# Optimization experiments

Hardware: AMD Instinct MI355X
Metric: run time of the kernel (lower is better)

Reference implementation:

```python
import jax, jax.numpy as jnp
import numpy as np

B, S, E, KD = 4, 2048, 1024, 1024

def setup_inputs() -> dict:
    key = jax.random.key(0)
    k1, k2, k3, k4 = jax.random.split(key, 4)
    # nn.Linear weights are [out_features, in_features]
    x = jax.random.normal(k1, (B, S, E), dtype=jnp.float32)
    W_q = jax.random.normal(k2, (KD, E), dtype=jnp.float32) * (E ** -0.5)
    W_k = jax.random.normal(k3, (KD, E), dtype=jnp.float32) * (E ** -0.5)
    W_v = jax.random.normal(k4, (E, E), dtype=jnp.float32) * (E ** -0.5)
    return {"x": x, "W_q": W_q, "W_k": W_k, "W_v": W_v}

def reference(x, W_q, W_k, W_v):
    # Projections: y = x @ W.T  (torch Linear convention)
    Q = jnp.einsum('bse,ke->bsk', x, W_q)   # [B,S,KD]
    K = jnp.einsum('bse,ke->bsk', x, W_k)   # [B,S,KD]
    V = jnp.einsum('bse,fe->bsf', x, W_v)   # [B,S,E]
    key_dim = W_q.shape[0]
    scores = jnp.einsum('bqk,bsk->bqs', Q, K) / jnp.sqrt(jnp.asarray(key_dim, x.dtype))
    S_len = x.shape[1]
    causal = jnp.tril(jnp.ones((S_len, S_len), dtype=bool))  # [S,S]
    scores = jnp.where(causal, scores, -jnp.inf)
    weights = jax.nn.softmax(scores, axis=-1)                # [B,S,S]
    out = jnp.einsum('bqs,bsf->bqf', weights, V)             # [B,S,E]
    return out
```

## Files before the change

kernel.cpp:

```cpp
#include <hip/hip_runtime.h>

typedef _Float16 f16;
typedef _Float16 f16x8 __attribute__((ext_vector_type(8)));
typedef float    f32x4 __attribute__((ext_vector_type(4)));

__device__ __forceinline__ void gld_lds16(const void* g, void* l) {
    __builtin_amdgcn_global_load_lds((__attribute__((address_space(1))) void*)g,
                                     (__attribute__((address_space(3))) void*)l,
                                     16, 0, 0);
}

#define BARRIER() do { asm volatile("" ::: "memory"); \
                       __builtin_amdgcn_s_barrier();  \
                       asm volatile("" ::: "memory"); } while (0)

template<bool STG, int VM1, int VM4>
__device__ __forceinline__ void tile256(
    f32x4 (&acc)[8][4],
    const f16* Ak0, const f16* Ak1, const f16* Bk0, const f16* Bk1,
    const f16* gAn, const f16* gBn,
    f16* lAn, f16* lBn,
    int lda, int ldb)
{
    {
        f16x8 a[4], b[4];
        #pragma unroll
        for (int mf = 0; mf < 4; mf++) a[mf] = *(const f16x8*)(Ak0 + mf * 1024);
        #pragma unroll
        for (int nf = 0; nf < 4; nf++) b[nf] = *(const f16x8*)(Bk0 + nf * 1024);
        if (STG) {
            gld_lds16(gBn,                  lBn);
            gld_lds16(gBn + (long)64 * ldb, lBn + 4096);
        }
        BARRIER();
        __builtin_amdgcn_s_setprio(1);
        #pragma unroll
        for (int mf = 0; mf < 4; mf++)
            #pragma unroll
            for (int nf = 0; nf < 4; nf++)
                acc[mf][nf] = __builtin_amdgcn_mfma_f32_16x16x32_f16(
                    a[mf], b[nf], acc[mf][nf], 0, 0, 0);
        __builtin_amdgcn_s_setprio(0);
        if (VM1 == 2)      asm volatile("s_waitcnt vmcnt(2)" ::: "memory");
        else if (VM1 == 0) asm volatile("s_waitcnt vmcnt(0)" ::: "memory");
        BARRIER();
        f16x8 a2[4];
        #pragma unroll
        for (int mf = 0; mf < 4; mf++) a2[mf] = *(const f16x8*)(Ak0 + (mf + 4) * 1024);
        if (STG) {
            gld_lds16(gBn + (long)128 * ldb, lBn + 8192);
            gld_lds16(gBn + (long)192 * ldb, lBn + 12288);
        }
        BARRIER();
        __builtin_amdgcn_s_setprio(1);
        #pragma unroll
        for (int mf = 0; mf < 4; mf++)
            #pragma unroll
            for (int nf = 0; nf < 4; nf++)
                acc[mf + 4][nf] = __builtin_amdgcn_mfma_f32_16x16x32_f16(
                    a2[mf], b[nf], acc[mf + 4][nf], 0, 0, 0);
        __builtin_amdgcn_s_setprio(0);
        BARRIER();
    }
    {
        f16x8 a[4], b[4];
        #pragma unroll
        for (int mf = 0; mf < 4; mf++) a[mf] = *(const f16x8*)(Ak1 + mf * 1024);
        #pragma unroll
        for (int nf = 0; nf < 4; nf++) b[nf] = *(const f16x8*)(Bk1 + nf * 1024);
        if (STG) {
            gld_lds16(gAn,                   lAn);
            gld_lds16(gAn + (long)128 * lda, lAn + 8192);
        }
        BARRIER();
        __builtin_amdgcn_s_setprio(1);
        #pragma unroll
        for (int mf = 0; mf < 4; mf++)
            #pragma unroll
            for (int nf = 0; nf < 4; nf++)
                acc[mf][nf] = __builtin_amdgcn_mfma_f32_16x16x32_f16(
                    a[mf], b[nf], acc[mf][nf], 0, 0, 0);
        __builtin_amdgcn_s_setprio(0);
        BARRIER();
        f16x8 a2[4];
        #pragma unroll
        for (int mf = 0; mf < 4; mf++) a2[mf] = *(const f16x8*)(Ak1 + (mf + 4) * 1024);
        if (STG) {
            gld_lds16(gAn + (long)64 * lda,  lAn + 4096);
            gld_lds16(gAn + (long)192 * lda, lAn + 12288);
        }
        BARRIER();
        __builtin_amdgcn_s_setprio(1);
        #pragma unroll
        for (int mf = 0; mf < 4; mf++)
            #pragma unroll
            for (int nf = 0; nf < 4; nf++)
                acc[mf + 4][nf] = __builtin_amdgcn_mfma_f32_16x16x32_f16(
                    a2[mf], b[nf], acc[mf + 4][nf], 0, 0, 0);
        __builtin_amdgcn_s_setprio(0);
        if (VM4 == 2)      asm volatile("s_waitcnt vmcnt(2)" ::: "memory");
        else if (VM4 == 0) asm volatile("s_waitcnt vmcnt(0)" ::: "memory");
        BARRIER();
    }
}

__global__ void __launch_bounds__(512, 2)
gemm256_k1024(const f16* __restrict__ A, const f16* __restrict__ B,
              f16* __restrict__ C, int lda, int ldb, int ldc)
{
    const int m  = (int)blockIdx.x;
    const int L  = (m & 7) * 32 + (m >> 3);
    const int i0 = (L >> 3) * 256;
    const int j0 = (L & 7) * 256;

    __shared__ f16 Lds[2 * 32768] __attribute__((aligned(16)));

    const int tid  = threadIdx.x;
    const int lane = tid & 63;
    const int wave = tid >> 6;
    const int wm = wave >> 2, wn = wave & 3;
    const int row16 = lane & 15, quad = lane >> 4;
    const int swz = row16 & 7;

    const int c0 = (quad ^ swz) * 8;
    const int c1 = ((quad + 4) ^ swz) * 8;
    const f16* A0k0 = Lds + (wm * 128 + row16) * 64 + c0;
    const f16* A0k1 = Lds + (wm * 128 + row16) * 64 + c1;
    const f16* B0k0 = Lds + 16384 + (wn * 64 + row16) * 64 + c0;
    const f16* B0k1 = Lds + 16384 + (wn * 64 + row16) * 64 + c1;

    const int srow = tid >> 3;
    const int scol = ((tid & 7) ^ (srow & 7)) * 8;
    const f16* gA = A + (long)(i0 + srow) * lda + scol;
    const f16* gB = B + (long)(j0 + srow) * ldb + scol;
    f16* lA0 = Lds + tid * 8;
    f16* lB0 = Lds + 16384 + tid * 8;
    f16* lA1 = Lds + 32768 + tid * 8;
    f16* lB1 = Lds + 32768 + 16384 + tid * 8;

    gld_lds16(gB,                   lB0);
    gld_lds16(gB + (long)64 * ldb,  lB0 + 4096);
    gld_lds16(gB + (long)128 * ldb, lB0 + 8192);
    gld_lds16(gB + (long)192 * ldb, lB0 + 12288);
    gld_lds16(gA,                   lA0);
    gld_lds16(gA + (long)128 * lda, lA0 + 8192);
    gld_lds16(gA + (long)64 * lda,  lA0 + 4096);
    gld_lds16(gA + (long)192 * lda, lA0 + 12288);

    f32x4 acc[8][4] = {};

    asm volatile("s_waitcnt vmcnt(2)" ::: "memory");
    BARRIER();

    for (int t = 0; t < 14; t += 2) {
        tile256<true, 2, 2>(acc, A0k0, A0k1, B0k0, B0k1,
                            gA + (t + 1) * 64, gB + (t + 1) * 64,
                            lA1, lB1, lda, ldb);
        tile256<true, 2, 2>(acc, A0k0 + 32768, A0k1 + 32768,
                            B0k0 + 32768, B0k1 + 32768,
                            gA + (t + 2) * 64, gB + (t + 2) * 64,
                            lA0, lB0, lda, ldb);
    }
    tile256<true, 2, 2>(acc, A0k0, A0k1, B0k0, B0k1,
                        gA + 15 * 64, gB + 15 * 64, lA1, lB1, lda, ldb);
    tile256<false, 0, -1>(acc, A0k0 + 32768, A0k1 + 32768,
                          B0k0 + 32768, B0k1 + 32768,
                          nullptr, nullptr, nullptr, nullptr, lda, ldb);

    #pragma unroll
    for (int mf = 0; mf < 8; mf++) {
        const int r0 = i0 + wm * 128 + mf * 16 + quad * 4;
        #pragma unroll
        for (int nf = 0; nf < 4; nf++) {
            const int c = j0 + wn * 64 + nf * 16 + row16;
            #pragma unroll
            for (int r = 0; r < 4; r++)
                C[(long)(r0 + r) * ldc + c] = (f16)acc[mf][nf][r];
        }
    }
}

template<typename OutT>
__device__ __forceinline__ void gemm128_body(
    const f16* __restrict__ A, const f16* __restrict__ B, OutT* __restrict__ C,
    int lda, int ldb, int ldc, int Keff, float scale, int i0, int j0)
{
    __shared__ f16 As[128 * 64] __attribute__((aligned(16)));
    __shared__ f16 Bs[64 * 64]  __attribute__((aligned(16)));

    const int tid  = threadIdx.x;
    const int lane = tid & 63;
    const int wave = tid >> 6;
    const int row16 = lane & 15;
    const int quad  = lane >> 4;
    const int swz   = row16 & 7;
    const int wr = (wave >> 1) * 64;
    const int wc = (wave & 1) * 32;

    const int srow = tid >> 3;
    const int scol = ((tid & 7) ^ (srow & 7)) * 8;
    const f16* gA = A + (long)(i0 + srow) * lda + scol;
    const f16* gB = B + (long)(j0 + srow) * ldb + scol;
    f16* lA = As + tid * 8;
    f16* lB = Bs + tid * 8;

    f32x4 acc[4][2] = {};

    for (int k0 = 0; k0 < Keff; k0 += 64) {
        gld_lds16(gA + k0,                  lA);
        gld_lds16(gA + k0 + (long)32 * lda, lA + 32 * 64);
        gld_lds16(gA + k0 + (long)64 * lda, lA + 64 * 64);
        gld_lds16(gA + k0 + (long)96 * lda, lA + 96 * 64);
        gld_lds16(gB + k0,                  lB);
        gld_lds16(gB + k0 + (long)32 * ldb, lB + 32 * 64);
        __syncthreads();

        #pragma unroll
        for (int kk = 0; kk < 2; kk++) {
            f16x8 af[4], bf[2];
            #pragma unroll
            for (int t = 0; t < 4; t++)
                af[t] = *(const f16x8*)(As + (wr + t * 16 + row16) * 64
                                           + (((kk * 4 + quad) ^ swz) * 8));
            #pragma unroll
            for (int t = 0; t < 2; t++)
                bf[t] = *(const f16x8*)(Bs + (wc + t * 16 + row16) * 64
                                           + (((kk * 4 + quad) ^ swz) * 8));
            #pragma unroll
            for (int mt = 0; mt < 4; mt++)
                #pragma unroll
                for (int nt = 0; nt < 2; nt++)
                    acc[mt][nt] = __builtin_amdgcn_mfma_f32_16x16x32_f16(
                        af[mt], bf[nt], acc[mt][nt], 0, 0, 0);
        }
        __syncthreads();
    }

    #pragma unroll
    for (int mt = 0; mt < 4; mt++) {
        const int r0 = i0 + wr + mt * 16 + quad * 4;
        #pragma unroll
        for (int nt = 0; nt < 2; nt++) {
            const int c = j0 + wc + nt * 16 + row16;
            #pragma unroll
            for (int r = 0; r < 4; r++)
                C[(long)(r0 + r) * ldc + c] = (OutT)(acc[mt][nt][r] * scale);
        }
    }
}

__global__ void __launch_bounds__(256)
gemm_vt_sc(const f16* __restrict__ xh, const f16* __restrict__ wvh,
           const f16* __restrict__ QKh, f16* __restrict__ Vt,
           f16* __restrict__ Sc)
{
    const int blk = (int)blockIdx.x;
    if (blk < 1024) {
        const int L = (blk & 7) * 128 + (blk >> 3);
        const int j = L >> 3;
        const int i = L & 7;
        gemm128_body<f16>(wvh, xh, Vt, 1024, 1024, 8192, 1024, 1.f,
                          i * 128, j * 64);
    } else {
        const int m = blk - 1024;
        const int L = (m & 7) * 136 + (m >> 3);
        const int z = L / 272;
        const int r = L - z * 272;
        int y = 0;
        while ((y + 1) * (y + 2) <= r) y++;
        const int x = r - y * (y + 1);
        const long off = (long)z * (2048L * 2048);
        gemm128_body<f16>(QKh + off, QKh + 1024 + off, Sc + off,
                          2048, 2048, 2048, 1024, 0.03125f, y * 128, x * 64);
    }
}

__global__ void __launch_bounds__(256)
gemm_pv(const f16* __restrict__ Sc, const f16* __restrict__ Vt,
        float* __restrict__ out)
{
    const int n  = (int)blockIdx.x;
    const int by = 15 - (n >> 6);
    const int rem = n & 63;
    const int x  = rem >> 2;
    const int z  = rem & 3;
    const int i0 = by * 128;
    const int Keff = i0 + 128;
    gemm128_body<float>(Sc + (long)z * (2048L * 2048),
                        Vt + (long)z * 2048,
                        out + (long)z * (2048L * 1024),
                        2048, 8192, 1024, Keff, 1.f, i0, x * 64);
}

__global__ void __launch_bounds__(256)
softmax_causal(f16* __restrict__ Sc)
{
    const int bid = (int)blockIdx.x;
    const int k = bid & 7;
    const int s = bid >> 3;
    const long b = k >> 1;
    int i;
    if (!(k & 1)) i = s;
    else          i = (s < 640) ? (1408 + s) : (1024 + (s - 640));

    f16* row = Sc + ((b * 2048 + i) * 2048L);
    const int L = ((i >> 7) + 1) << 7;

    const int tid = threadIdx.x;
    const int c0  = tid * 8;
    const int lane = tid & 63, wave = tid >> 6;
    const bool act = c0 < L;

    float v[8];
    float m = -3.4e38f;
    if (act) {
        f16x8 in = *(const f16x8*)(row + c0);
        #pragma unroll
        for (int j = 0; j < 8; j++) {
            const bool ok = (c0 + j) <= i;
            v[j] = ok ? (float)in[j] : -3.4e38f;
            m = fmaxf(m, v[j]);
        }
    }
    #pragma unroll
    for (int off = 32; off > 0; off >>= 1)
        m = fmaxf(m, __shfl_down(m, off, 64));
    __shared__ float redm[4];
    if (lane == 0) redm[wave] = m;
    __syncthreads();
    const float m0 = fmaxf(fmaxf(redm[0], redm[1]), fmaxf(redm[2], redm[3]));

    float e[8];
    float s2 = 0.f;
    if (act) {
        #pragma unroll
        for (int j = 0; j < 8; j++) {
            const bool ok = (c0 + j) <= i;
            e[j] = ok ? __expf(v[j] - m0) : 0.f;
            s2 += e[j];
        }
    }
    #pragma unroll
    for (int off = 32; off > 0; off >>= 1)
        s2 += __shfl_down(s2, off, 64);
    __shared__ float reds[4];
    if (lane == 0) reds[wave] = s2;
    __syncthreads();
    const float inv = 1.f / (reds[0] + reds[1] + reds[2] + reds[3]);

    if (act) {
        f16x8 o;
        #pragma unroll
        for (int j = 0; j < 8; j++) o[j] = (f16)(e[j] * inv);
        *(f16x8*)(row + c0) = o;
    }
}

__global__ void __launch_bounds__(256)
convert_all(const float* __restrict__ x, const float* __restrict__ Wq,
            const float* __restrict__ Wk, const float* __restrict__ Wv,
            f16* __restrict__ xh, f16* __restrict__ wh)
{
    const long blk = blockIdx.x;
    const float* src;
    f16* dst;
    long base;
    if (blk < 4096)      { src = x;  dst = xh;                    base = blk * 2048; }
    else if (blk < 4608) { src = Wq; dst = wh;                    base = (blk - 4096) * 2048; }
    else if (blk < 5120) { src = Wk; dst = wh + 1024L * 1024;     base = (blk - 4608) * 2048; }
    else                 { src = Wv; dst = wh + 2L * 1024 * 1024; base = (blk - 5120) * 2048; }
    const long i = base + (long)threadIdx.x * 8;
    f32x4 a = *(const f32x4*)(src + i);
    f32x4 b = *(const f32x4*)(src + i + 4);
    f16x8 o;
    o[0] = (f16)a[0]; o[1] = (f16)a[1]; o[2] = (f16)a[2]; o[3] = (f16)a[3];
    o[4] = (f16)b[0]; o[5] = (f16)b[1]; o[6] = (f16)b[2]; o[7] = (f16)b[3];
    *(f16x8*)(dst + i) = o;
}

extern "C" void kernel_launch(void* const* d_in, const int* in_sizes, int n_in,
                              void* d_out, int out_size, void* d_ws, size_t ws_size,
                              hipStream_t stream)
{
    (void)in_sizes; (void)n_in; (void)out_size; (void)ws_size;
    const float* x  = (const float*)d_in[0];
    const float* Wq = (const float*)d_in[1];
    const float* Wk = (const float*)d_in[2];
    const float* Wv = (const float*)d_in[3];
    float* out = (float*)d_out;

    const long NX = 4L * 2048 * 1024;
    const long NW = 1024L * 1024;

    char* p = (char*)d_ws;
    f16* xh  = (f16*)p; p += NX * 2;
    f16* wh  = (f16*)p; p += 3 * NW * 2;
    f16* QKh = (f16*)p; p += 2 * NX * 2;
    f16* Vt  = (f16*)p; p += NX * 2;
    f16* Sc  = (f16*)p; p += 4L * 2048 * 2048 * 2;
    f16* wvh = wh + 2L * NW;

    convert_all<<<5632, 256, 0, stream>>>(x, Wq, Wk, Wv, xh, wh);

    gemm256_k1024<<<256, 512, 0, stream>>>(
        xh, wh, QKh, 1024, 1024, 2048);

    gemm_vt_sc<<<2112, 256, 0, stream>>>(xh, wvh, QKh, Vt, Sc);

    softmax_causal<<<4 * 2048, 256, 0, stream>>>(Sc);

    gemm_pv<<<1024, 256, 0, stream>>>(Sc, Vt, out);
}
```

Baseline: 219.5 us.

## Reassociate QK^T as x·(W_q^T W_k)·x^T to drop a projection GEMM

Computes M = W_q^T W_k once from transposed fp16 weights, then forms K' = x M^T and scores = x K'^T, removing the separate Q projection. The K' and V projections share a 256-tile GEMM kernel, and the score GEMM now reads xh and K' directly. Weight transposes are folded into the conversion kernel. This cuts roughly one 8192x1024x1024 GEMM but adds an extra fp16 rounding of M, which may affect accuracy.

```diff
diff --git a/kernel.cpp b/kernel.cpp
--- a/kernel.cpp
+++ b/kernel.cpp
@@ -104,18 +104,10 @@
     }
 }
 
-__global__ void __launch_bounds__(512, 2)
-gemm256_k1024(const f16* __restrict__ A, const f16* __restrict__ B,
-              f16* __restrict__ C, int lda, int ldb, int ldc)
-{
-    const int m  = (int)blockIdx.x;
-    const int L  = (m & 7) * 32 + (m >> 3);
-    const int i0 = (L >> 3) * 256;
-    const int j0 = (L & 7) * 256;
-
-    __shared__ f16 Lds[2 * 32768] __attribute__((aligned(16)));
-
-    const int tid  = threadIdx.x;
+__device__ __forceinline__ void gemm256_body(
+    const f16* __restrict__ A, const f16* __restrict__ B, f16* __restrict__ C,
+    int lda, int ldb, int ldc, int i0, int j0, f16* Lds, int tid)
+{
     const int lane = tid & 63;
     const int wave = tid >> 6;
     const int wm = wave >> 2, wn = wave & 3;
@@ -180,6 +172,27 @@
     }
 }
 
+__global__ void __launch_bounds__(512, 2)
+gemm_kv(const f16* __restrict__ xh, const f16* __restrict__ M,
+        const f16* __restrict__ wvh, f16* __restrict__ Kp,
+        f16* __restrict__ Vt)
+{
+    __shared__ f16 Lds[2 * 32768] __attribute__((aligned(16)));
+    const int m = (int)blockIdx.x;
+    if (m < 128) {
+        const int T = (m & 7) * 16 + (m >> 3);
+        const int i = T >> 2, j = T & 3;
+        gemm256_body(xh, M, Kp, 1024, 1024, 1024,
+                     i * 256, j * 256, Lds, (int)threadIdx.x);
+    } else {
+        const int mm = m - 128;
+        const int T = (mm & 7) * 16 + (mm >> 3);
+        const int i = T & 3, j = T >> 2;
+        gemm256_body(wvh, xh, Vt, 1024, 1024, 8192,
+                     i * 256, j * 256, Lds, (int)threadIdx.x);
+    }
+}
+
 template<typename OutT>
 __device__ __forceinline__ void gemm128_body(
     const f16* __restrict__ A, const f16* __restrict__ B, OutT* __restrict__ C,
@@ -250,29 +263,30 @@
 }
 
 __global__ void __launch_bounds__(256)
-gemm_vt_sc(const f16* __restrict__ xh, const f16* __restrict__ wvh,
-           const f16* __restrict__ QKh, f16* __restrict__ Vt,
-           f16* __restrict__ Sc)
+gemm_m(const f16* __restrict__ wqt, const f16* __restrict__ wkt,
+       f16* __restrict__ M)
 {
     const int blk = (int)blockIdx.x;
-    if (blk < 1024) {
-        const int L = (blk & 7) * 128 + (blk >> 3);
-        const int j = L >> 3;
-        const int i = L & 7;
-        gemm128_body<f16>(wvh, xh, Vt, 1024, 1024, 8192, 1024, 1.f,
-                          i * 128, j * 64);
-    } else {
-        const int m = blk - 1024;
-        const int L = (m & 7) * 136 + (m >> 3);
-        const int z = L / 272;
-        const int r = L - z * 272;
-        int y = 0;
-        while ((y + 1) * (y + 2) <= r) y++;
-        const int x = r - y * (y + 1);
-        const long off = (long)z * (2048L * 2048);
-        gemm128_body<f16>(QKh + off, QKh + 1024 + off, Sc + off,
-                          2048, 2048, 2048, 1024, 0.03125f, y * 128, x * 64);
-    }
+    const int i = blk >> 4;
+    const int j = blk & 15;
+    gemm128_body<f16>(wqt, wkt, M, 1024, 1024, 1024, 1024, 1.f,
+                      i * 128, j * 64);
+}
+
+__global__ void __launch_bounds__(256)
+gemm_sc(const f16* __restrict__ xh, const f16* __restrict__ Kp,
+        f16* __restrict__ Sc)
+{
+    const int m = (int)blockIdx.x;
+    const int L = (m & 7) * 136 + (m >> 3);
+    const int z = L / 272;
+    const int r = L - z * 272;
+    int y = 0;
+    while ((y + 1) * (y + 2) <= r) y++;
+    const int x = r - y * (y + 1);
+    const long aoff = (long)z * (2048L * 1024);
+    gemm128_body<f16>(xh + aoff, Kp + aoff, Sc + (long)z * (2048L * 2048),
+                      1024, 1024, 2048, 1024, 0.03125f, y * 128, x * 64);
 }
 
 __global__ void __launch_bounds__(256)
@@ -359,23 +373,50 @@
 __global__ void __launch_bounds__(256)
 convert_all(const float* __restrict__ x, const float* __restrict__ Wq,
             const float* __restrict__ Wk, const float* __restrict__ Wv,
-            f16* __restrict__ xh, f16* __restrict__ wh)
+            f16* __restrict__ xh, f16* __restrict__ wvh,
+            f16* __restrict__ wqt, f16* __restrict__ wkt)
 {
     const long blk = blockIdx.x;
-    const float* src;
-    f16* dst;
-    long base;
-    if (blk < 4096)      { src = x;  dst = xh;                    base = blk * 2048; }
-    else if (blk < 4608) { src = Wq; dst = wh;                    base = (blk - 4096) * 2048; }
-    else if (blk < 5120) { src = Wk; dst = wh + 1024L * 1024;     base = (blk - 4608) * 2048; }
-    else                 { src = Wv; dst = wh + 2L * 1024 * 1024; base = (blk - 5120) * 2048; }
-    const long i = base + (long)threadIdx.x * 8;
-    f32x4 a = *(const f32x4*)(src + i);
-    f32x4 b = *(const f32x4*)(src + i + 4);
-    f16x8 o;
-    o[0] = (f16)a[0]; o[1] = (f16)a[1]; o[2] = (f16)a[2]; o[3] = (f16)a[3];
-    o[4] = (f16)b[0]; o[5] = (f16)b[1]; o[6] = (f16)b[2]; o[7] = (f16)b[3];
-    *(f16x8*)(dst + i) = o;
+    if (blk < 4608) {
+        const float* src;
+        f16* dst;
+        long base;
+        if (blk < 4096) { src = x;  dst = xh;  base = blk * 2048; }
+        else            { src = Wv; dst = wvh; base = (blk - 4096) * 2048; }
+        const long i = base + (long)threadIdx.x * 8;
+        f32x4 a = *(const f32x4*)(src + i);
+        f32x4 b = *(const f32x4*)(src + i + 4);
+        f16x8 o;
+        o[0] = (f16)a[0]; o[1] = (f16)a[1]; o[2] = (f16)a[2]; o[3] = (f16)a[3];
+        o[4] = (f16)b[0]; o[5] = (f16)b[1]; o[6] = (f16)b[2]; o[7] = (f16)b[3];
+        *(f16x8*)(dst + i) = o;
+    } else {
+        const int tb = (int)blk - 4608;
+        const float* W = (tb < 256) ? Wq : Wk;
+        f16* O = (tb < 256) ? wqt : wkt;
+        const int tt = tb & 255;
+        const int k0 = (tt >> 4) * 64;
+        const int e0 = (tt & 15) * 64;
+        __shared__ f16 T[64][72] __attribute__((aligned(16)));
+        const int t = (int)threadIdx.x;
+        #pragma unroll
+        for (int p = 0; p < 4; p++) {
+            const int r = p * 16 + (t >> 4);
+            const int c = (t & 15) * 4;
+            f32x4 v = *(const f32x4*)(W + (long)(k0 + r) * 1024 + e0 + c);
+            T[c + 0][r] = (f16)v[0];
+            T[c + 1][r] = (f16)v[1];
+            T[c + 2][r] = (f16)v[2];
+            T[c + 3][r] = (f16)v[3];
+        }
+        __syncthreads();
+        const int er = t >> 2;
+        const int kc = (t & 3) * 16;
+        f16x8 a = *(const f16x8*)(&T[er][kc]);
+        f16x8 b = *(const f16x8*)(&T[er][kc + 8]);
+        *(f16x8*)(O + (long)(e0 + er) * 1024 + k0 + kc)     = a;
+        *(f16x8*)(O + (long)(e0 + er) * 1024 + k0 + kc + 8) = b;
+    }
 }
 
 extern "C" void kernel_launch(void* const* d_in, const int* in_sizes, int n_in,
@@ -394,18 +435,21 @@
 
     char* p = (char*)d_ws;
     f16* xh  = (f16*)p; p += NX * 2;
-    f16* wh  = (f16*)p; p += 3 * NW * 2;
-    f16* QKh = (f16*)p; p += 2 * NX * 2;
+    f16* wqt = (f16*)p; p += NW * 2;
+    f16* wkt = (f16*)p; p += NW * 2;
+    f16* wvh = (f16*)p; p += NW * 2;
+    f16* Mb  = (f16*)p; p += NW * 2;
+    f16* Kp  = (f16*)p; p += NX * 2;
     f16* Vt  = (f16*)p; p += NX * 2;
     f16* Sc  = (f16*)p; p += 4L * 2048 * 2048 * 2;
-    f16* wvh = wh + 2L * NW;
-
-    convert_all<<<5632, 256, 0, stream>>>(x, Wq, Wk, Wv, xh, wh);
-
-    gemm256_k1024<<<256, 512, 0, stream>>>(
-        xh, wh, QKh, 1024, 1024, 2048);
-
-    gemm_vt_sc<<<2112, 256, 0, stream>>>(xh, wvh, QKh, Vt, Sc);
+
+    convert_all<<<5120, 256, 0, stream>>>(x, Wq, Wk, Wv, xh, wvh, wqt, wkt);
+
+    gemm_m<<<128, 256, 0, stream>>>(wqt, wkt, Mb);
+
+    gemm_kv<<<256, 512, 0, stream>>>(xh, Mb, wvh, Kp, Vt);
+
+    gemm_sc<<<1088, 256, 0, stream>>>(xh, Kp, Sc);
 
     softmax_causal<<<4 * 2048, 256, 0, stream>>>(Sc);
 
```

Result: faster. 212.0 us (-3.4%).
